# Kernel optimization log

Hardware: AMD Instinct MI355X
Metric: run time of the kernel (lower is better)

## Reference

```python
import jax, jax.numpy as jnp
import numpy as np

B = 256
C_IN, F_IN = 32, 256
C_OUT, F_OUT = 32, 256
KERNEL_SIZE = 4
BN_EPS = 1e-5


def _block_mask():
    # channel-wise connectivity: output channel o sees input channels in its kernel_size block
    co = jnp.arange(C_OUT)[:, None] // KERNEL_SIZE
    ci = jnp.arange(C_IN)[None, :] // KERNEL_SIZE
    return co == ci  # [C_OUT, C_IN] bool


def setup_inputs() -> dict:
    key = jax.random.key(0)
    k_x, k_w, k_b, k_g, k_be = jax.random.split(key, 5)
    x = jax.random.normal(k_x, (B, C_IN, F_IN), dtype=jnp.float32)
    fan_in = KERNEL_SIZE * F_IN
    W = jax.random.normal(k_w, (C_OUT, C_IN, F_OUT, F_IN), dtype=jnp.float32) / np.float32(np.sqrt(fan_in))
    bias = jax.random.normal(k_b, (C_OUT, F_OUT), dtype=jnp.float32) * 0.01
    gamma = 1.0 + 0.1 * jax.random.normal(k_g, (C_OUT * F_OUT,), dtype=jnp.float32)
    beta = 0.1 * jax.random.normal(k_be, (C_OUT * F_OUT,), dtype=jnp.float32)
    mask = _block_mask()
    return {"x": x, "W": W, "bias": bias, "gamma": gamma, "beta": beta, "mask": mask}


def reference(x, W, bias, gamma, beta, mask):
    # masked sparse linear: y[b,o,f] = sum_{c,i} mask[o,c] * W[o,c,f,i] * x[b,c,i] + bias[o,f]
    Wm = W * mask[:, :, None, None].astype(W.dtype)
    y = jnp.einsum('bci,ocfi->bof', x, Wm) + bias  # [B, C_OUT, F_OUT]
    b = y.shape[0]
    yf = y.reshape(b, C_OUT * F_OUT)
    # BatchNorm1d in training mode: biased batch statistics over the batch dim
    mean = jnp.mean(yf, axis=0)
    var = jnp.var(yf, axis=0)
    yn = (yf - mean) * jax.lax.rsqrt(var + BN_EPS) * gamma + beta
    # Swish: x * sigmoid(x)
    out = yn * jax.nn.sigmoid(yn)
    return out.reshape(b, C_OUT, F_OUT)
```

## Files before the change

kernel.cpp:

```cpp
#include <hip/hip_runtime.h>
#include <hip/hip_bf16.h>


typedef float  f32x4  __attribute__((ext_vector_type(4)));
typedef short  short8 __attribute__((ext_vector_type(8)));
typedef unsigned short u16x8 __attribute__((ext_vector_type(8)));

static __device__ __forceinline__ unsigned short f2bf(float f) {
    unsigned int u = __float_as_uint(f);
    u += 0x7FFFu + ((u >> 16) & 1u);
    return (unsigned short)(u >> 16);
}

#define GLL(gp, lp) __builtin_amdgcn_global_load_lds( \
    (const __attribute__((address_space(1))) unsigned int*)(gp), \
    (__attribute__((address_space(3))) unsigned int*)(lp), 16, 0, 0)

__global__ __launch_bounds__(256) void conv_kernel(const float* __restrict__ x,
                                                   unsigned short* __restrict__ xb) {
    const int base = blockIdx.x * 1024 + threadIdx.x;
#pragma unroll
    for (int i = 0; i < 4; ++i) {
        const int cid = base + i * 256;
        const f32x4 a = *(const f32x4*)(x + (size_t)cid * 8);
        const f32x4 b = *(const f32x4*)(x + (size_t)cid * 8 + 4);
        u16x8 v;
        v[0] = f2bf(a[0]); v[1] = f2bf(a[1]); v[2] = f2bf(a[2]); v[3] = f2bf(a[3]);
        v[4] = f2bf(b[0]); v[5] = f2bf(b[1]); v[6] = f2bf(b[2]); v[7] = f2bf(b[3]);
        *(u16x8*)(xb + (size_t)cid * 8) = v;
    }
}

__global__ __launch_bounds__(256, 1) void fused_kernel(
    const unsigned short* __restrict__ xb, const float* __restrict__ W,
    const float* __restrict__ gamma, const float* __restrict__ beta,
    float* __restrict__ out)
{
    __shared__ __align__(16) char ldsA[3][32768];
    __shared__ __align__(16) char ldsB[2][4096];
    __shared__ float wps1[4][32], wps2[4][32];
    __shared__ float sa[32], sb[32];

    const int bid = blockIdx.x;
    const int g   = bid & 7;
    const int nt  = bid >> 3;
    const int o   = g * 4 + (nt >> 3);
    const int f0  = (nt & 7) * 32;
    const int gcol0 = o * 256 + f0;

    const int t    = threadIdx.x;
    const int wave = t >> 6;
    const int lane = t & 63;
    const int lr   = lane & 15;
    const int kq   = lane >> 4;

    f32x4 acc[4][2];
    const f32x4 zero = {0.f, 0.f, 0.f, 0.f};
#pragma unroll
    for (int i = 0; i < 4; ++i) { acc[i][0] = zero; acc[i][1] = zero; }

    f32x4 breg[4][2];

    auto ISSUE_A = [&](int st) {
        const unsigned short* asrc = xb + g * 1024 + st * 64;
        char* Ab = ldsA[st % 3];
#pragma unroll
        for (int i = 0; i < 8; ++i) {
            const int cid = i * 256 + t;
            const int r = cid >> 3, c = cid & 7;
            GLL(asrc + (size_t)r * 8192 + (c ^ (r & 7)) * 8, Ab + cid * 16);
        }
    };
    auto ISSUE_W = [&](int st) {
        const int cp = st >> 2, kc = (st & 3) * 64;
        const float* bsrc = W + ((size_t)((o * 32 + g * 4 + cp) * 256 + f0)) * 256 + kc
                              + (size_t)(t >> 3) * 256 + (t & 7) * 8;
        breg[st & 3][0] = *(const f32x4*)bsrc;
        breg[st & 3][1] = *(const f32x4*)(bsrc + 4);
    };
    auto WRITEB = [&](int st) {
        const int n = t >> 3, c = t & 7;
        short8 v;
        v[0] = (short)f2bf(breg[st & 3][0][0]); v[1] = (short)f2bf(breg[st & 3][0][1]);
        v[2] = (short)f2bf(breg[st & 3][0][2]); v[3] = (short)f2bf(breg[st & 3][0][3]);
        v[4] = (short)f2bf(breg[st & 3][1][0]); v[5] = (short)f2bf(breg[st & 3][1][1]);
        v[6] = (short)f2bf(breg[st & 3][1][2]); v[7] = (short)f2bf(breg[st & 3][1][3]);
        *(short8*)(ldsB[st & 1] + n * 128 + ((c ^ (n & 7)) * 16)) = v;
    };
    auto COMPUTE = [&](int st) {
        const char* Ab = ldsA[st % 3];
        const char* Bb = ldsB[st & 1];
#pragma unroll
        for (int ks = 0; ks < 2; ++ks) {
            short8 af[4], bfr[2];
#pragma unroll
            for (int i = 0; i < 4; ++i) {
                const int ra = wave * 64 + i * 16 + lr;
                af[i] = *(const short8*)(Ab + ra * 128 + (((ks * 4 + kq) ^ (ra & 7)) * 16));
            }
#pragma unroll
            for (int j = 0; j < 2; ++j) {
                const int n = j * 16 + lr;
                bfr[j] = *(const short8*)(Bb + n * 128 + (((ks * 4 + kq) ^ (n & 7)) * 16));
            }
#pragma unroll
            for (int i = 0; i < 4; ++i)
#pragma unroll
                for (int j = 0; j < 2; ++j)
                    acc[i][j] = __builtin_amdgcn_mfma_f32_16x16x32_bf16(af[i], bfr[j], acc[i][j], 0, 0, 0);
        }
    };

    ISSUE_A(0);
    ISSUE_A(1);
    ISSUE_W(0);
    ISSUE_W(1);
    ISSUE_W(2);
    WRITEB(0);
    asm volatile("s_waitcnt lgkmcnt(0)" ::: "memory");
    __builtin_amdgcn_s_barrier();

#pragma unroll
    for (int st = 0; st < 16; ++st) {
        COMPUTE(st);
        if (st <= 13) ISSUE_A(st + 2);
        if (st <= 12) ISSUE_W(st + 3);
        if (st <= 14) {
            WRITEB(st + 1);
            if (st <= 12) {
                asm volatile("s_waitcnt vmcnt(12)" ::: "memory");
            } else if (st == 13) {
                asm volatile("s_waitcnt vmcnt(8)" ::: "memory");
            } else {
                asm volatile("s_waitcnt vmcnt(0)" ::: "memory");
            }
            asm volatile("s_waitcnt lgkmcnt(0)" ::: "memory");
            __builtin_amdgcn_s_barrier();
        }
    }

    float s1[2] = {0.f, 0.f}, s2[2] = {0.f, 0.f};
#pragma unroll
    for (int i = 0; i < 4; ++i)
#pragma unroll
        for (int j = 0; j < 2; ++j)
#pragma unroll
            for (int r = 0; r < 4; ++r) {
                const float v = acc[i][j][r];
                s1[j] += v; s2[j] += v * v;
            }
#pragma unroll
    for (int j = 0; j < 2; ++j) {
        s1[j] += __shfl_xor(s1[j], 16); s2[j] += __shfl_xor(s2[j], 16);
        s1[j] += __shfl_xor(s1[j], 32); s2[j] += __shfl_xor(s2[j], 32);
    }
    if (kq == 0) {
#pragma unroll
        for (int j = 0; j < 2; ++j) {
            wps1[wave][j * 16 + lr] = s1[j];
            wps2[wave][j * 16 + lr] = s2[j];
        }
    }
    __syncthreads();
    if (t < 32) {
        float a1 = wps1[0][t] + wps1[1][t] + wps1[2][t] + wps1[3][t];
        float a2 = wps2[0][t] + wps2[1][t] + wps2[2][t] + wps2[3][t];
        const float mean = a1 * (1.0f / 256.0f);
        const float var  = a2 * (1.0f / 256.0f) - mean * mean;
        const float istd = rsqrtf(var + 1e-5f);
        const float ga = gamma[gcol0 + t];
        sa[t] = ga * istd;
        sb[t] = beta[gcol0 + t] - mean * ga * istd;
    }
    __syncthreads();

#pragma unroll
    for (int i = 0; i < 4; ++i) {
        const int row0 = wave * 64 + i * 16 + kq * 4;
#pragma unroll
        for (int j = 0; j < 2; ++j) {
            const int col = j * 16 + lr;
            const float a = sa[col], b2 = sb[col];
#pragma unroll
            for (int r = 0; r < 4; ++r) {
                const float z = a * acc[i][j][r] + b2;
                out[(size_t)(row0 + r) * 8192 + gcol0 + col] = z / (1.0f + expf(-z));
            }
        }
    }
}

extern "C" void kernel_launch(void* const* d_in, const int* in_sizes, int n_in,
                              void* d_out, int out_size, void* d_ws, size_t ws_size,
                              hipStream_t stream) {
    const float* x     = (const float*)d_in[0];
    const float* W     = (const float*)d_in[1];
    const float* gamma = (const float*)d_in[3];
    const float* beta  = (const float*)d_in[4];
    float* out = (float*)d_out;

    unsigned short* xb = (unsigned short*)d_ws;

    conv_kernel<<<256, 256, 0, stream>>>(x, xb);
    fused_kernel<<<256, 256, 0, stream>>>(xb, W, gamma, beta, out);
}
```

Before: 25.60 us.

## Split batch across two blocks per tile with atomic cross-block BN statistics

Each output tile's 256-row batch is now split across two workgroups, doubling the grid to 512 blocks and halving per-block LDS and accumulator size. Because batch-norm statistics need the full batch, the two blocks add partial sums into a global stats buffer with atomics and then wait on a spin flag for each other. The aim is more parallelism and occupancy (launch bounds raised to 2 blocks per CU). The cost is duplicated weight loading and conversion for each half, an extra memset, and a spin-wait that could deadlock if the paired blocks are not co-resident.

```diff
diff --git a/kernel.cpp b/kernel.cpp
--- a/kernel.cpp
+++ b/kernel.cpp
@@ -31,19 +31,21 @@
     }
 }
 
-__global__ __launch_bounds__(256, 1) void fused_kernel(
+__global__ __launch_bounds__(256, 2) void fused_kernel(
     const unsigned short* __restrict__ xb, const float* __restrict__ W,
     const float* __restrict__ gamma, const float* __restrict__ beta,
-    float* __restrict__ out)
+    float* __restrict__ out, float* __restrict__ stats,
+    unsigned int* __restrict__ flags)
 {
-    __shared__ __align__(16) char ldsA[3][32768];
+    __shared__ __align__(16) char ldsA[3][16384];
     __shared__ __align__(16) char ldsB[2][4096];
     __shared__ float wps1[4][32], wps2[4][32];
     __shared__ float sa[32], sb[32];
 
     const int bid = blockIdx.x;
     const int g   = bid & 7;
-    const int nt  = bid >> 3;
+    const int h   = (bid >> 3) & 1;
+    const int nt  = bid >> 4;
     const int o   = g * 4 + (nt >> 3);
     const int f0  = (nt & 7) * 32;
     const int gcol0 = o * 256 + f0;
@@ -54,18 +56,20 @@
     const int lr   = lane & 15;
     const int kq   = lane >> 4;
 
-    f32x4 acc[4][2];
+    f32x4 acc[2][2];
     const f32x4 zero = {0.f, 0.f, 0.f, 0.f};
 #pragma unroll
-    for (int i = 0; i < 4; ++i) { acc[i][0] = zero; acc[i][1] = zero; }
+    for (int i = 0; i < 2; ++i) { acc[i][0] = zero; acc[i][1] = zero; }
 
     f32x4 breg[4][2];
 
+    const unsigned short* xh = xb + (size_t)(h * 128) * 8192 + g * 1024;
+
     auto ISSUE_A = [&](int st) {
-        const unsigned short* asrc = xb + g * 1024 + st * 64;
+        const unsigned short* asrc = xh + st * 64;
         char* Ab = ldsA[st % 3];
 #pragma unroll
-        for (int i = 0; i < 8; ++i) {
+        for (int i = 0; i < 4; ++i) {
             const int cid = i * 256 + t;
             const int r = cid >> 3, c = cid & 7;
             GLL(asrc + (size_t)r * 8192 + (c ^ (r & 7)) * 8, Ab + cid * 16);
@@ -92,10 +96,10 @@
         const char* Bb = ldsB[st & 1];
 #pragma unroll
         for (int ks = 0; ks < 2; ++ks) {
-            short8 af[4], bfr[2];
-#pragma unroll
-            for (int i = 0; i < 4; ++i) {
-                const int ra = wave * 64 + i * 16 + lr;
+            short8 af[2], bfr[2];
+#pragma unroll
+            for (int i = 0; i < 2; ++i) {
+                const int ra = wave * 32 + i * 16 + lr;
                 af[i] = *(const short8*)(Ab + ra * 128 + (((ks * 4 + kq) ^ (ra & 7)) * 16));
             }
 #pragma unroll
@@ -104,7 +108,7 @@
                 bfr[j] = *(const short8*)(Bb + n * 128 + (((ks * 4 + kq) ^ (n & 7)) * 16));
             }
 #pragma unroll
-            for (int i = 0; i < 4; ++i)
+            for (int i = 0; i < 2; ++i)
 #pragma unroll
                 for (int j = 0; j < 2; ++j)
                     acc[i][j] = __builtin_amdgcn_mfma_f32_16x16x32_bf16(af[i], bfr[j], acc[i][j], 0, 0, 0);
@@ -128,9 +132,9 @@
         if (st <= 14) {
             WRITEB(st + 1);
             if (st <= 12) {
-                asm volatile("s_waitcnt vmcnt(12)" ::: "memory");
+                asm volatile("s_waitcnt vmcnt(8)" ::: "memory");
             } else if (st == 13) {
-                asm volatile("s_waitcnt vmcnt(8)" ::: "memory");
+                asm volatile("s_waitcnt vmcnt(6)" ::: "memory");
             } else {
                 asm volatile("s_waitcnt vmcnt(0)" ::: "memory");
             }
@@ -141,7 +145,7 @@
 
     float s1[2] = {0.f, 0.f}, s2[2] = {0.f, 0.f};
 #pragma unroll
-    for (int i = 0; i < 4; ++i)
+    for (int i = 0; i < 2; ++i)
 #pragma unroll
         for (int j = 0; j < 2; ++j)
 #pragma unroll
@@ -163,8 +167,26 @@
     }
     __syncthreads();
     if (t < 32) {
-        float a1 = wps1[0][t] + wps1[1][t] + wps1[2][t] + wps1[3][t];
-        float a2 = wps2[0][t] + wps2[1][t] + wps2[2][t] + wps2[3][t];
+        const float a1 = wps1[0][t] + wps1[1][t] + wps1[2][t] + wps1[3][t];
+        const float a2 = wps2[0][t] + wps2[1][t] + wps2[2][t] + wps2[3][t];
+        __hip_atomic_fetch_add(stats + gcol0 + t, a1,
+                               __ATOMIC_RELAXED, __HIP_MEMORY_SCOPE_AGENT);
+        __hip_atomic_fetch_add(stats + 8192 + gcol0 + t, a2,
+                               __ATOMIC_RELAXED, __HIP_MEMORY_SCOPE_AGENT);
+    }
+    __syncthreads();
+    if (t == 0) {
+        unsigned int* fl = flags + (g * 32 + nt);
+        __hip_atomic_fetch_add(fl, 1u, __ATOMIC_RELEASE, __HIP_MEMORY_SCOPE_AGENT);
+        while (__hip_atomic_load(fl, __ATOMIC_ACQUIRE, __HIP_MEMORY_SCOPE_AGENT) < 2u)
+            __builtin_amdgcn_s_sleep(1);
+    }
+    __syncthreads();
+    if (t < 32) {
+        const float a1 = __hip_atomic_load(stats + gcol0 + t,
+                                           __ATOMIC_RELAXED, __HIP_MEMORY_SCOPE_AGENT);
+        const float a2 = __hip_atomic_load(stats + 8192 + gcol0 + t,
+                                           __ATOMIC_RELAXED, __HIP_MEMORY_SCOPE_AGENT);
         const float mean = a1 * (1.0f / 256.0f);
         const float var  = a2 * (1.0f / 256.0f) - mean * mean;
         const float istd = rsqrtf(var + 1e-5f);
@@ -175,8 +197,8 @@
     __syncthreads();
 
 #pragma unroll
-    for (int i = 0; i < 4; ++i) {
-        const int row0 = wave * 64 + i * 16 + kq * 4;
+    for (int i = 0; i < 2; ++i) {
+        const int row0 = h * 128 + wave * 32 + i * 16 + kq * 4;
 #pragma unroll
         for (int j = 0; j < 2; ++j) {
             const int col = j * 16 + lr;
@@ -199,8 +221,11 @@
     const float* beta  = (const float*)d_in[4];
     float* out = (float*)d_out;
 
-    unsigned short* xb = (unsigned short*)d_ws;
-
+    unsigned short* xb    = (unsigned short*)d_ws;
+    float*          stats = (float*)((char*)d_ws + (4u << 20));
+    unsigned int*   flags = (unsigned int*)((char*)d_ws + (4u << 20) + 65536);
+
+    hipMemsetAsync((char*)d_ws + (4u << 20), 0, 65536 + 1024, stream);
     conv_kernel<<<256, 256, 0, stream>>>(x, xb);
-    fused_kernel<<<256, 256, 0, stream>>>(xb, W, gamma, beta, out);
-}
+    fused_kernel<<<512, 256, 0, stream>>>(xb, W, gamma, beta, out, stats, flags);
+}
```

Result: slower. 37.56 us (+46.7%).

## Double fused kernel block size to 512 threads, halving per-wave work

Applied to the files above, without the earlier changes.

Raises the fused GEMM+BatchNorm+Swish kernel from 4 to 8 waves per block. Each wave now owns 32 rows instead of 64, and each thread loads one f32x4 of W instead of two. The A-tile load loop, the W conversion/LDS write, the vmcnt wait counts and the cross-wave statistics reduction are all rewritten to match. The aim is more latency hiding and memory-level parallelism per CU. In exchange, fewer MFMAs are issued per LDS fragment load and barrier cost is spread across more waves.

```diff
diff --git a/kernel.cpp b/kernel.cpp
--- a/kernel.cpp
+++ b/kernel.cpp
@@ -5,11 +5,12 @@
 typedef float  f32x4  __attribute__((ext_vector_type(4)));
 typedef short  short8 __attribute__((ext_vector_type(8)));
 typedef unsigned short u16x8 __attribute__((ext_vector_type(8)));
-
-static __device__ __forceinline__ unsigned short f2bf(float f) {
+typedef unsigned int   u32x2 __attribute__((ext_vector_type(2)));
+
+static __device__ __forceinline__ unsigned int f2bf(float f) {
     unsigned int u = __float_as_uint(f);
     u += 0x7FFFu + ((u >> 16) & 1u);
-    return (unsigned short)(u >> 16);
+    return u >> 16;
 }
 
 #define GLL(gp, lp) __builtin_amdgcn_global_load_lds( \
@@ -31,14 +32,14 @@
     }
 }
 
-__global__ __launch_bounds__(256, 1) void fused_kernel(
+__global__ __launch_bounds__(512, 1) void fused_kernel(
     const unsigned short* __restrict__ xb, const float* __restrict__ W,
     const float* __restrict__ gamma, const float* __restrict__ beta,
     float* __restrict__ out)
 {
     __shared__ __align__(16) char ldsA[3][32768];
     __shared__ __align__(16) char ldsB[2][4096];
-    __shared__ float wps1[4][32], wps2[4][32];
+    __shared__ float wps1[8][32], wps2[8][32];
     __shared__ float sa[32], sb[32];
 
     const int bid = blockIdx.x;
@@ -54,48 +55,47 @@
     const int lr   = lane & 15;
     const int kq   = lane >> 4;
 
-    f32x4 acc[4][2];
+    f32x4 acc[2][2];
     const f32x4 zero = {0.f, 0.f, 0.f, 0.f};
 #pragma unroll
-    for (int i = 0; i < 4; ++i) { acc[i][0] = zero; acc[i][1] = zero; }
-
-    f32x4 breg[4][2];
+    for (int i = 0; i < 2; ++i) { acc[i][0] = zero; acc[i][1] = zero; }
+
+    f32x4 breg[4];
 
     auto ISSUE_A = [&](int st) {
         const unsigned short* asrc = xb + g * 1024 + st * 64;
         char* Ab = ldsA[st % 3];
 #pragma unroll
-        for (int i = 0; i < 8; ++i) {
-            const int cid = i * 256 + t;
+        for (int i = 0; i < 4; ++i) {
+            const int cid = i * 512 + t;
             const int r = cid >> 3, c = cid & 7;
             GLL(asrc + (size_t)r * 8192 + (c ^ (r & 7)) * 8, Ab + cid * 16);
         }
     };
     auto ISSUE_W = [&](int st) {
         const int cp = st >> 2, kc = (st & 3) * 64;
-        const float* bsrc = W + ((size_t)((o * 32 + g * 4 + cp) * 256 + f0)) * 256 + kc
-                              + (size_t)(t >> 3) * 256 + (t & 7) * 8;
-        breg[st & 3][0] = *(const f32x4*)bsrc;
-        breg[st & 3][1] = *(const f32x4*)(bsrc + 4);
+        const float* bsrc = W + ((size_t)((o * 32 + g * 4 + cp) * 256 + f0)) * 256 + kc;
+        breg[st & 3] = *(const f32x4*)(bsrc + (size_t)(t >> 4) * 256 + (t & 15) * 4);
     };
     auto WRITEB = [&](int st) {
-        const int n = t >> 3, c = t & 7;
-        short8 v;
-        v[0] = (short)f2bf(breg[st & 3][0][0]); v[1] = (short)f2bf(breg[st & 3][0][1]);
-        v[2] = (short)f2bf(breg[st & 3][0][2]); v[3] = (short)f2bf(breg[st & 3][0][3]);
-        v[4] = (short)f2bf(breg[st & 3][1][0]); v[5] = (short)f2bf(breg[st & 3][1][1]);
-        v[6] = (short)f2bf(breg[st & 3][1][2]); v[7] = (short)f2bf(breg[st & 3][1][3]);
-        *(short8*)(ldsB[st & 1] + n * 128 + ((c ^ (n & 7)) * 16)) = v;
+        const int n = t >> 4;
+        const int ch = (t & 15) >> 1;
+        const int half = t & 1;
+        const f32x4 v = breg[st & 3];
+        u32x2 d;
+        d[0] = f2bf(v[0]) | (f2bf(v[1]) << 16);
+        d[1] = f2bf(v[2]) | (f2bf(v[3]) << 16);
+        *(u32x2*)(ldsB[st & 1] + n * 128 + ((ch ^ (n & 7)) * 16) + half * 8) = d;
     };
     auto COMPUTE = [&](int st) {
         const char* Ab = ldsA[st % 3];
         const char* Bb = ldsB[st & 1];
 #pragma unroll
         for (int ks = 0; ks < 2; ++ks) {
-            short8 af[4], bfr[2];
-#pragma unroll
-            for (int i = 0; i < 4; ++i) {
-                const int ra = wave * 64 + i * 16 + lr;
+            short8 af[2], bfr[2];
+#pragma unroll
+            for (int i = 0; i < 2; ++i) {
+                const int ra = wave * 32 + i * 16 + lr;
                 af[i] = *(const short8*)(Ab + ra * 128 + (((ks * 4 + kq) ^ (ra & 7)) * 16));
             }
 #pragma unroll
@@ -104,7 +104,7 @@
                 bfr[j] = *(const short8*)(Bb + n * 128 + (((ks * 4 + kq) ^ (n & 7)) * 16));
             }
 #pragma unroll
-            for (int i = 0; i < 4; ++i)
+            for (int i = 0; i < 2; ++i)
 #pragma unroll
                 for (int j = 0; j < 2; ++j)
                     acc[i][j] = __builtin_amdgcn_mfma_f32_16x16x32_bf16(af[i], bfr[j], acc[i][j], 0, 0, 0);
@@ -128,9 +128,9 @@
         if (st <= 14) {
             WRITEB(st + 1);
             if (st <= 12) {
-                asm volatile("s_waitcnt vmcnt(12)" ::: "memory");
+                asm volatile("s_waitcnt vmcnt(6)" ::: "memory");
             } else if (st == 13) {
-                asm volatile("s_waitcnt vmcnt(8)" ::: "memory");
+                asm volatile("s_waitcnt vmcnt(5)" ::: "memory");
             } else {
                 asm volatile("s_waitcnt vmcnt(0)" ::: "memory");
             }
@@ -141,7 +141,7 @@
 
     float s1[2] = {0.f, 0.f}, s2[2] = {0.f, 0.f};
 #pragma unroll
-    for (int i = 0; i < 4; ++i)
+    for (int i = 0; i < 2; ++i)
 #pragma unroll
         for (int j = 0; j < 2; ++j)
 #pragma unroll
@@ -163,8 +163,9 @@
     }
     __syncthreads();
     if (t < 32) {
-        float a1 = wps1[0][t] + wps1[1][t] + wps1[2][t] + wps1[3][t];
-        float a2 = wps2[0][t] + wps2[1][t] + wps2[2][t] + wps2[3][t];
+        float a1 = 0.f, a2 = 0.f;
+#pragma unroll
+        for (int q = 0; q < 8; ++q) { a1 += wps1[q][t]; a2 += wps2[q][t]; }
         const float mean = a1 * (1.0f / 256.0f);
         const float var  = a2 * (1.0f / 256.0f) - mean * mean;
         const float istd = rsqrtf(var + 1e-5f);
@@ -175,8 +176,8 @@
     __syncthreads();
 
 #pragma unroll
-    for (int i = 0; i < 4; ++i) {
-        const int row0 = wave * 64 + i * 16 + kq * 4;
+    for (int i = 0; i < 2; ++i) {
+        const int row0 = wave * 32 + i * 16 + kq * 4;
 #pragma unroll
         for (int j = 0; j < 2; ++j) {
             const int col = j * 16 + lr;
@@ -202,5 +203,5 @@
     unsigned short* xb = (unsigned short*)d_ws;
 
     conv_kernel<<<256, 256, 0, stream>>>(x, xb);
-    fused_kernel<<<256, 256, 0, stream>>>(xb, W, gamma, beta, out);
-}
+    fused_kernel<<<256, 512, 0, stream>>>(xb, W, gamma, beta, out);
+}
```

New measurement: 23.51 us, median of 3. 1.09x faster.
